# Kernel optimization log

Measured on AMD Instinct MI355X. Metric: run time of the kernel, lower is better.

Reference implementation:

```python
import jax, jax.numpy as jnp
import numpy as np

# Profile-HMM forward-backward in log space.
# inputs : (M, B, L, S) soft/one-hot observation features
# log_A  : (M, Q, Q) row-stochastic log transition matrix
# log_pi : (M, Q)    log initial distribution
# log_B  : (M, Q, S) log emission matrix

M, B, L, Q, S = 1, 64, 2048, 256, 26
EPS = 1e-16


def setup_inputs() -> dict:
    key = jax.random.key(0)
    k1, k2, k3, k4 = jax.random.split(key, 4)
    inputs = jax.random.uniform(k1, (M, B, L, S), dtype=jnp.float32)
    log_A = jax.nn.log_softmax(jax.random.normal(k2, (M, Q, Q), dtype=jnp.float32), axis=-1)
    log_pi = jax.nn.log_softmax(jax.random.normal(k3, (M, Q), dtype=jnp.float32), axis=-1)
    log_B = jax.nn.log_softmax(jax.random.normal(k4, (M, Q, S), dtype=jnp.float32), axis=-1)
    return {"inputs": inputs, "log_A": log_A, "log_pi": log_pi, "log_B": log_B}


def _forward_backward(inputs, log_A, log_pi, log_B):
    # emission probs per state: e[m,b,l,q] = sum_s inputs[m,b,l,s] * B[m,q,s]
    emit = jnp.einsum('mbls,mqs->mblq', inputs, jnp.exp(log_B))
    log_e = jnp.log(emit + EPS)
    log_e_t = jnp.moveaxis(log_e, 2, 0)  # (L, M, B, Q) time-major

    # forward recursion: alpha_t[i] = logsumexp_j(alpha_{t-1}[j] + A[j,i]) + e_t[i]
    alpha0 = log_pi[:, None, :] + log_e_t[0]  # (M, B, Q)

    def fstep(alpha, le):
        new = jax.nn.logsumexp(alpha[..., :, None] + log_A[:, None], axis=-2) + le
        return new, new

    _, alphas = jax.lax.scan(fstep, alpha0, log_e_t[1:])
    alphas = jnp.concatenate([alpha0[None], alphas], axis=0)  # (L, M, B, Q)

    # backward recursion: beta_t[i] = logsumexp_j(A[i,j] + e_{t+1}[j] + beta_{t+1}[j])
    beta_last = jnp.zeros_like(alpha0)

    def bstep(beta, le):
        new = jax.nn.logsumexp(log_A[:, None] + (le + beta)[:, :, None, :], axis=-1)
        return new, new

    _, betas = jax.lax.scan(bstep, beta_last, log_e_t[1:], reverse=True)
    betas = jnp.concatenate([betas, beta_last[None]], axis=0)  # (L, M, B, Q)

    loglik = jax.nn.logsumexp(alphas[-1], axis=-1)  # (M, B)
    post = alphas + betas - loglik[None, :, :, None]  # state posterior log probs
    return jnp.moveaxis(post, 0, 2), loglik  # (M, B, L, Q), (M, B)


def reference(inputs, log_A, log_pi, log_B):
    post, loglik = _forward_backward(inputs, log_A, log_pi, log_B)
    return post, loglik
```

## Files before the change

### kernel.cpp

```cpp
#include <hip/hip_runtime.h>

namespace {

constexpr int B = 64;
constexpr int L = 2048;
constexpr int Q = 256;
constexpr int S = 26;
constexpr float EPS = 1e-16f;
constexpr size_t POST = (size_t)B * L * Q;

typedef _Float16 h2 __attribute__((ext_vector_type(2)));

union U16 {
  uint4 u;
  h2 h[4];
};

struct Smem {
  alignas(16) _Float16 vb[2][Q];
  alignas(16) float rowbuf[2][32];
  float sh[2];
  alignas(16) float afin[Q];
};

__device__ __forceinline__ float wave_max64(float x) {
#pragma unroll
  for (int off = 32; off > 0; off >>= 1) x = fmaxf(x, __shfl_xor(x, off, 64));
  return x;
}
__device__ __forceinline__ float wave_sum64(float x) {
#pragma unroll
  for (int off = 32; off > 0; off >>= 1) x += __shfl_xor(x, off, 64);
  return x;
}

__device__ __forceinline__ float emit_row(const float* __restrict__ rb,
                                          const float* __restrict__ eB) {
  const float4* r4 = (const float4*)rb;
  float4 c0 = r4[0], c1 = r4[1], c2 = r4[2], c3 = r4[3], c4 = r4[4], c5 = r4[5];
  float2 c6 = ((const float2*)rb)[12];
  float a0 = EPS, a1 = 0.f, a2 = 0.f, a3 = 0.f;
  a0 = fmaf(c0.x, eB[0], a0);  a1 = fmaf(c0.y, eB[1], a1);
  a2 = fmaf(c0.z, eB[2], a2);  a3 = fmaf(c0.w, eB[3], a3);
  a0 = fmaf(c1.x, eB[4], a0);  a1 = fmaf(c1.y, eB[5], a1);
  a2 = fmaf(c1.z, eB[6], a2);  a3 = fmaf(c1.w, eB[7], a3);
  a0 = fmaf(c2.x, eB[8], a0);  a1 = fmaf(c2.y, eB[9], a1);
  a2 = fmaf(c2.z, eB[10], a2); a3 = fmaf(c2.w, eB[11], a3);
  a0 = fmaf(c3.x, eB[12], a0); a1 = fmaf(c3.y, eB[13], a1);
  a2 = fmaf(c3.z, eB[14], a2); a3 = fmaf(c3.w, eB[15], a3);
  a0 = fmaf(c4.x, eB[16], a0); a1 = fmaf(c4.y, eB[17], a1);
  a2 = fmaf(c4.z, eB[18], a2); a3 = fmaf(c4.w, eB[19], a3);
  a0 = fmaf(c5.x, eB[20], a0); a1 = fmaf(c5.y, eB[21], a1);
  a2 = fmaf(c5.z, eB[22], a2); a3 = fmaf(c5.w, eB[23], a3);
  a0 = fmaf(c6.x, eB[24], a0); a1 = fmaf(c6.y, eB[25], a1);
  return (a0 + a1) + (a2 + a3);
}

__device__ __forceinline__ float matvec_f16(const h2* __restrict__ Af,
                                            const _Float16* __restrict__ vrow) {
  const uint4* v4 = (const uint4*)vrow;
  float acc[8] = {0.f, 0.f, 0.f, 0.f, 0.f, 0.f, 0.f, 0.f};
#pragma unroll
  for (int c = 0; c < 16; ++c) {
    U16 u;
    u.u = v4[c];
#pragma unroll
    for (int k = 0; k < 4; ++k) {
      const int j = 4 * c + k;
      acc[j & 7] = __builtin_amdgcn_fdot2(u.h[k], Af[j], acc[j & 7], false);
    }
  }
  float s = ((acc[0] + acc[1]) + (acc[2] + acc[3])) +
            ((acc[4] + acc[5]) + (acc[6] + acc[7]));
  return s + __shfl_xor(s, 32, 64);
}

__device__ __forceinline__ void fwd_impl(int b, const float* __restrict__ inputs,
                                         const float* __restrict__ log_A,
                                         const float* __restrict__ log_pi,
                                         const float* __restrict__ log_B,
                                         float* __restrict__ out, Smem& sm) {
  const int tid = threadIdx.x, w = tid >> 6, lane = tid & 63;
  const int l31 = lane & 31;
  const bool lo = lane < 32;
  const int r = w * 32 + l31;
  const int jbase = lo ? 0 : 128;
  const bool stg = (w == 0) && (lane < 13);

  h2 Af[64];
#pragma unroll
  for (int k = 0; k < 64; ++k) {
    float x0 = __expf(log_A[(size_t)(jbase + 2 * k) * Q + r]);
    float x1 = __expf(log_A[(size_t)(jbase + 2 * k + 1) * Q + r]);
    Af[k] = h2{(_Float16)x0, (_Float16)x1};
  }
  float eB[S];
#pragma unroll
  for (int s = 0; s < S; ++s) eB[s] = __expf(log_B[r * S + s]);

  const float2* __restrict__ inp2 = (const float2*)(inputs + (size_t)b * L * S);
  float* __restrict__ post_b = out + (size_t)b * L * Q;

  if (stg) {
    float2 g0 = inp2[lane];
    float2 g1 = inp2[13 + lane];
    ((float2*)sm.rowbuf[1])[lane] = g0;
    ((float2*)sm.rowbuf[0])[lane] = g1;
  }
  __syncthreads();
  float emit0 = emit_row(sm.rowbuf[1], eB);
  float alpha_cur = __logf(emit0) + log_pi[r];
  if (tid == 0) sm.sh[0] = alpha_cur;
  __syncthreads();
  float rd_prev = sm.sh[0];
  if (lo) sm.vb[0][r] = (_Float16)__expf(alpha_cur - rd_prev);
  float alpha_prev = alpha_cur;
  __syncthreads();

  int p = 0;
  for (int t = 1; t < L; ++t) {
    const float rd = sm.sh[p];
    float2 g;
    const int tt = (t + 1 < L) ? t + 1 : L - 1;
    if (stg) g = inp2[(size_t)tt * 13 + lane];
    if (lo) post_b[(size_t)(t - 1) * Q + r] = alpha_prev;
    const float emit = emit_row(sm.rowbuf[p], eB);
    const float X = matvec_f16(Af, sm.vb[p] + jbase);
    const float z = X * emit;
    const float gam = __expf(rd_prev - rd);
    if (lo) sm.vb[p ^ 1][r] = (_Float16)(z * gam);
    alpha_cur = __logf(z) + rd_prev;
    if (tid == 0) sm.sh[p ^ 1] = alpha_cur;
    if (stg) ((float2*)sm.rowbuf[p ^ 1])[lane] = g;
    alpha_prev = alpha_cur;
    rd_prev = rd;
    __syncthreads();
    p ^= 1;
  }

  if (lo) post_b[(size_t)(L - 1) * Q + r] = alpha_prev;
  if (lo) sm.afin[r] = alpha_prev;
  __syncthreads();
  if (w == 0) {
    float4 fa = ((const float4*)sm.afin)[lane];
    float m = fmaxf(fmaxf(fa.x, fa.y), fmaxf(fa.z, fa.w));
    m = wave_max64(m);
    float ss = __expf(fa.x - m) + __expf(fa.y - m) + __expf(fa.z - m) + __expf(fa.w - m);
    ss = wave_sum64(ss);
    if (lane == 0) out[POST + b] = __logf(ss) + m;
  }
}

template <int MODE>
__device__ __forceinline__ void bwd_impl(int b, const float* __restrict__ inputs,
                                         const float* __restrict__ log_A,
                                         const float* __restrict__ log_B,
                                         float* __restrict__ out,
                                         float* __restrict__ ws, Smem& sm) {
  const int tid = threadIdx.x, w = tid >> 6, lane = tid & 63;
  const int l31 = lane & 31;
  const bool lo = lane < 32;
  const int r = w * 32 + l31;
  const int jbase = lo ? 0 : 128;
  const bool stg = (w == 0) && (lane < 13);

  h2 Af[64];
  {
    const float* row = log_A + (size_t)r * Q + jbase;
#pragma unroll
    for (int k = 0; k < 64; ++k) {
      float x0 = __expf(row[2 * k]);
      float x1 = __expf(row[2 * k + 1]);
      Af[k] = h2{(_Float16)x0, (_Float16)x1};
    }
  }
  float eB[S];
#pragma unroll
  for (int s = 0; s < S; ++s) eB[s] = __expf(log_B[r * S + s]);

  const float2* __restrict__ inp2 = (const float2*)(inputs + (size_t)b * L * S);
  float* __restrict__ post_b = out + (size_t)b * L * Q;
  float* __restrict__ ws_b = ws + (size_t)b * L * Q;

  float ll = 0.f, aprev_hold = 0.f;
  if (MODE == 1) {
    ll = out[POST + b];
    aprev_hold = post_b[(size_t)(L - 1) * Q + r];
  }

  if (stg) {
    float2 g0 = inp2[(size_t)(L - 1) * 13 + lane];
    float2 g1 = inp2[(size_t)(L - 2) * 13 + lane];
    ((float2*)sm.rowbuf[1])[lane] = g0;
    ((float2*)sm.rowbuf[0])[lane] = g1;
  }
  __syncthreads();
  float emitL = emit_row(sm.rowbuf[1], eB);
  if (tid == 0) sm.sh[0] = __logf(emitL);
  __syncthreads();
  float rd_prev = sm.sh[0];
  if (lo) sm.vb[0][r] = (_Float16)(emitL * __expf(-rd_prev));
  float beta_prev = 0.f;
  __syncthreads();

  int p = 0;
  for (int t = L - 2; t >= 0; --t) {
    const float rd = sm.sh[p];
    float2 g;
    const int tt = (t > 0) ? t - 1 : 0;
    if (stg) g = inp2[(size_t)tt * 13 + lane];
    float anext = 0.f;
    if (MODE == 0) {
      if (lo) ws_b[(size_t)(t + 1) * Q + r] = beta_prev;
    } else {
      if (lo) post_b[(size_t)(t + 1) * Q + r] = aprev_hold + beta_prev - ll;
      anext = post_b[(size_t)t * Q + r];
    }
    const float emit = emit_row(sm.rowbuf[p], eB);
    const float raw = matvec_f16(Af, sm.vb[p] + jbase);
    const float beta = __logf(raw) + rd_prev;
    const float z = raw * emit;
    const float gam = __expf(rd_prev - rd);
    if (lo) sm.vb[p ^ 1][r] = (_Float16)(z * gam);
    if (tid == 0) sm.sh[p ^ 1] = beta + __logf(emit);
    if (stg) ((float2*)sm.rowbuf[p ^ 1])[lane] = g;
    beta_prev = beta;
    rd_prev = rd;
    if (MODE == 1) aprev_hold = anext;
    __syncthreads();
    p ^= 1;
  }

  if (MODE == 0) {
    if (lo) ws_b[r] = beta_prev;
  } else {
    if (lo) post_b[r] = aprev_hold + beta_prev - ll;
  }
}

__global__ __launch_bounds__(512, 1)
void hmm_fwdbwd(const float* __restrict__ inputs, const float* __restrict__ log_A,
                const float* __restrict__ log_pi, const float* __restrict__ log_B,
                float* __restrict__ out, float* __restrict__ ws) {
  __shared__ Smem sm;
  if (blockIdx.x < B) fwd_impl(blockIdx.x, inputs, log_A, log_pi, log_B, out, sm);
  else                bwd_impl<0>(blockIdx.x - B, inputs, log_A, log_B, out, ws, sm);
}

__global__ __launch_bounds__(256)
void hmm_combine(const float* __restrict__ ws, float* __restrict__ out) {
  const size_t idx = (size_t)blockIdx.x * 256 + threadIdx.x;
  const int b = (int)(idx >> 17);
  const float ll = out[POST + b];
  float4 a = ((const float4*)out)[idx];
  const float4 be = ((const float4*)ws)[idx];
  a.x += be.x - ll;
  a.y += be.y - ll;
  a.z += be.z - ll;
  a.w += be.w - ll;
  ((float4*)out)[idx] = a;
}

__global__ __launch_bounds__(512, 1)
void hmm_fwd_only(const float* __restrict__ inputs, const float* __restrict__ log_A,
                  const float* __restrict__ log_pi, const float* __restrict__ log_B,
                  float* __restrict__ out) {
  __shared__ Smem sm;
  fwd_impl(blockIdx.x, inputs, log_A, log_pi, log_B, out, sm);
}

__global__ __launch_bounds__(512, 1)
void hmm_bwd_fused(const float* __restrict__ inputs, const float* __restrict__ log_A,
                   const float* __restrict__ log_B, float* __restrict__ out) {
  __shared__ Smem sm;
  bwd_impl<1>(blockIdx.x, inputs, log_A, log_B, out, nullptr, sm);
}

}

extern "C" void kernel_launch(void* const* d_in, const int* in_sizes, int n_in,
                              void* d_out, int out_size, void* d_ws, size_t ws_size,
                              hipStream_t stream) {
  const float* inputs = (const float*)d_in[0];
  const float* log_A  = (const float*)d_in[1];
  const float* log_pi = (const float*)d_in[2];
  const float* log_B  = (const float*)d_in[3];
  float* out = (float*)d_out;
  float* ws  = (float*)d_ws;

  if (ws_size >= POST * sizeof(float)) {
    hipLaunchKernelGGL(hmm_fwdbwd, dim3(2 * B), dim3(512), 0, stream,
                       inputs, log_A, log_pi, log_B, out, ws);
    hipLaunchKernelGGL(hmm_combine, dim3((unsigned)(POST / 4 / 256)), dim3(256), 0, stream,
                       ws, out);
  } else {
    hipLaunchKernelGGL(hmm_fwd_only, dim3(B), dim3(512), 0, stream,
                       inputs, log_A, log_pi, log_B, out);
    hipLaunchKernelGGL(hmm_bwd_fused, dim3(B), dim3(512), 0, stream,
                       inputs, log_A, log_B, out);
  }
}
```

Baseline: 1.758 ms.

## Move per-step matvec and emission dot products onto MFMA matrix cores

Replaces the per-lane fdot2 transition matvec and the scalar emission dot product with 16x16x32 f16 MFMA instructions. Each wave now handles 32 states as two 16-column tiles, with only one row of the A operand populated. The emission product uses a hi/lo f16 split to keep near-fp32 accuracy. Launch bounds are raised to two blocks per CU. This trades a wasteful MFMA (only one of 16 rows useful) and extra fragment reads from LDS for shorter per-step latency on the serial recurrence. f16 rounding of the observation inputs also adds some accuracy risk.

```diff
diff --git a/kernel.cpp b/kernel.cpp
--- a/kernel.cpp
+++ b/kernel.cpp
@@ -10,15 +10,15 @@
 constexpr size_t POST = (size_t)B * L * Q;
 
 typedef _Float16 h2 __attribute__((ext_vector_type(2)));
-
-union U16 {
-  uint4 u;
-  h2 h[4];
-};
+typedef _Float16 f16x8 __attribute__((ext_vector_type(8)));
+typedef float f32x4 __attribute__((ext_vector_type(4)));
+
+#define MFMA16(a, b, c) __builtin_amdgcn_mfma_f32_16x16x32_f16((a), (b), (c), 0, 0, 0)
 
 struct Smem {
   alignas(16) _Float16 vb[2][Q];
-  alignas(16) float rowbuf[2][32];
+  alignas(16) _Float16 rowh[2][32];
+  alignas(16) _Float16 rowl[2][32];
   float sh[2];
   alignas(16) float afin[Q];
 };
@@ -34,45 +34,71 @@
   return x;
 }
 
-__device__ __forceinline__ float emit_row(const float* __restrict__ rb,
-                                          const float* __restrict__ eB) {
-  const float4* r4 = (const float4*)rb;
-  float4 c0 = r4[0], c1 = r4[1], c2 = r4[2], c3 = r4[3], c4 = r4[4], c5 = r4[5];
-  float2 c6 = ((const float2*)rb)[12];
-  float a0 = EPS, a1 = 0.f, a2 = 0.f, a3 = 0.f;
-  a0 = fmaf(c0.x, eB[0], a0);  a1 = fmaf(c0.y, eB[1], a1);
-  a2 = fmaf(c0.z, eB[2], a2);  a3 = fmaf(c0.w, eB[3], a3);
-  a0 = fmaf(c1.x, eB[4], a0);  a1 = fmaf(c1.y, eB[5], a1);
-  a2 = fmaf(c1.z, eB[6], a2);  a3 = fmaf(c1.w, eB[7], a3);
-  a0 = fmaf(c2.x, eB[8], a0);  a1 = fmaf(c2.y, eB[9], a1);
-  a2 = fmaf(c2.z, eB[10], a2); a3 = fmaf(c2.w, eB[11], a3);
-  a0 = fmaf(c3.x, eB[12], a0); a1 = fmaf(c3.y, eB[13], a1);
-  a2 = fmaf(c3.z, eB[14], a2); a3 = fmaf(c3.w, eB[15], a3);
-  a0 = fmaf(c4.x, eB[16], a0); a1 = fmaf(c4.y, eB[17], a1);
-  a2 = fmaf(c4.z, eB[18], a2); a3 = fmaf(c4.w, eB[19], a3);
-  a0 = fmaf(c5.x, eB[20], a0); a1 = fmaf(c5.y, eB[21], a1);
-  a2 = fmaf(c5.z, eB[22], a2); a3 = fmaf(c5.w, eB[23], a3);
-  a0 = fmaf(c6.x, eB[24], a0); a1 = fmaf(c6.y, eB[25], a1);
-  return (a0 + a1) + (a2 + a3);
-}
-
-__device__ __forceinline__ float matvec_f16(const h2* __restrict__ Af,
-                                            const _Float16* __restrict__ vrow) {
-  const uint4* v4 = (const uint4*)vrow;
-  float acc[8] = {0.f, 0.f, 0.f, 0.f, 0.f, 0.f, 0.f, 0.f};
-#pragma unroll
-  for (int c = 0; c < 16; ++c) {
-    U16 u;
-    u.u = v4[c];
-#pragma unroll
-    for (int k = 0; k < 4; ++k) {
-      const int j = 4 * c + k;
-      acc[j & 7] = __builtin_amdgcn_fdot2(u.h[k], Af[j], acc[j & 7], false);
-    }
-  }
-  float s = ((acc[0] + acc[1]) + (acc[2] + acc[3])) +
-            ((acc[4] + acc[5]) + (acc[6] + acc[7]));
-  return s + __shfl_xor(s, 32, 64);
+__device__ __forceinline__ void load_emit_frags(const float* __restrict__ log_B,
+                                                int c0, int c1, int g, int q,
+                                                f16x8& Bh0, f16x8& Bl0,
+                                                f16x8& Bh1, f16x8& Bl1) {
+#pragma unroll
+  for (int j = 0; j < 8; ++j) {
+    const int s = g * 8 + j;
+    const float v0 = (s < S) ? __expf(log_B[(size_t)(c0 + q) * S + s]) : 0.f;
+    const float v1 = (s < S) ? __expf(log_B[(size_t)(c1 + q) * S + s]) : 0.f;
+    const _Float16 h0 = (_Float16)v0, h1 = (_Float16)v1;
+    Bh0[j] = h0; Bl0[j] = (_Float16)(v0 - (float)h0);
+    Bh1[j] = h1; Bl1[j] = (_Float16)(v1 - (float)h1);
+  }
+}
+
+__device__ __forceinline__ void stage_row(Smem& sm, int buf, int lane, float2 gg) {
+  _Float16 ah = (_Float16)0.f, bh = (_Float16)0.f;
+  _Float16 al = (_Float16)0.f, bl = (_Float16)0.f;
+  if (lane < 13) {
+    ah = (_Float16)gg.x; bh = (_Float16)gg.y;
+    al = (_Float16)(gg.x - (float)ah);
+    bl = (_Float16)(gg.y - (float)bh);
+  }
+  ((h2*)sm.rowh[buf])[lane] = h2{ah, bh};
+  ((h2*)sm.rowl[buf])[lane] = h2{al, bl};
+}
+
+__device__ __forceinline__ void emit_mfma(const f16x8& xh, const f16x8& xl,
+                                          const f16x8& Bh0, const f16x8& Bl0,
+                                          const f16x8& Bh1, const f16x8& Bl1,
+                                          f32x4& E0, f32x4& E1) {
+  const f32x4 Z = {0.f, 0.f, 0.f, 0.f};
+  E0 = MFMA16(xh, Bl0, Z);
+  E0 = MFMA16(xl, Bh0, E0);
+  E0 = MFMA16(xh, Bh0, E0);
+  E1 = MFMA16(xh, Bl1, Z);
+  E1 = MFMA16(xl, Bh1, E1);
+  E1 = MFMA16(xh, Bh1, E1);
+}
+
+__device__ __forceinline__ void matvec_mfma(const f16x8* va, const f16x8* T0,
+                                            const f16x8* T1, float& x0, float& x1) {
+  const f32x4 Z = {0.f, 0.f, 0.f, 0.f};
+  f32x4 X0a = MFMA16(va[0], T0[0], Z);
+  f32x4 X1a = MFMA16(va[0], T1[0], Z);
+  f32x4 X0b = MFMA16(va[4], T0[4], Z);
+  f32x4 X1b = MFMA16(va[4], T1[4], Z);
+#pragma unroll
+  for (int f = 1; f < 4; ++f) {
+    X0a = MFMA16(va[f], T0[f], X0a);
+    X1a = MFMA16(va[f], T1[f], X1a);
+    X0b = MFMA16(va[f + 4], T0[f + 4], X0b);
+    X1b = MFMA16(va[f + 4], T1[f + 4], X1b);
+  }
+  x0 = X0a[0] + X0b[0];
+  x1 = X1a[0] + X1b[0];
+}
+
+__device__ __forceinline__ void read_frags(Smem& sm, int p, int g,
+                                           f16x8& xh, f16x8& xl, f16x8* va) {
+  xh = *(const f16x8*)(sm.rowh[p] + g * 8);
+  xl = *(const f16x8*)(sm.rowl[p] + g * 8);
+  const _Float16* vbp = sm.vb[p];
+#pragma unroll
+  for (int f = 0; f < 8; ++f) va[f] = *(const f16x8*)(vbp + f * 32 + g * 8);
 }
 
 __device__ __forceinline__ void fwd_impl(int b, const float* __restrict__ inputs,
@@ -81,65 +107,103 @@
                                          const float* __restrict__ log_B,
                                          float* __restrict__ out, Smem& sm) {
   const int tid = threadIdx.x, w = tid >> 6, lane = tid & 63;
-  const int l31 = lane & 31;
-  const bool lo = lane < 32;
-  const int r = w * 32 + l31;
-  const int jbase = lo ? 0 : 128;
-  const bool stg = (w == 0) && (lane < 13);
-
-  h2 Af[64];
-#pragma unroll
-  for (int k = 0; k < 64; ++k) {
-    float x0 = __expf(log_A[(size_t)(jbase + 2 * k) * Q + r]);
-    float x1 = __expf(log_A[(size_t)(jbase + 2 * k + 1) * Q + r]);
-    Af[k] = h2{(_Float16)x0, (_Float16)x1};
-  }
-  float eB[S];
-#pragma unroll
-  for (int s = 0; s < S; ++s) eB[s] = __expf(log_B[r * S + s]);
+  const int g = lane >> 4, q = lane & 15;
+  const int c0 = w * 32, c1 = c0 + 16;
+  const bool rdl = (q == 0);
+  const bool epi = (lane < 16);
+  const bool stg = (w == 0) && (lane < 16);
+
+  f16x8 T0[8], T1[8];
+#pragma unroll
+  for (int f = 0; f < 8; ++f) {
+#pragma unroll
+    for (int j = 0; j < 8; ++j) {
+      const int k = f * 32 + g * 8 + j;
+      T0[f][j] = (_Float16)__expf(log_A[(size_t)k * Q + c0 + q]);
+      T1[f][j] = (_Float16)__expf(log_A[(size_t)k * Q + c1 + q]);
+    }
+  }
+  f16x8 Bh0, Bl0, Bh1, Bl1;
+  load_emit_frags(log_B, c0, c1, g, q, Bh0, Bl0, Bh1, Bl1);
 
   const float2* __restrict__ inp2 = (const float2*)(inputs + (size_t)b * L * S);
   float* __restrict__ post_b = out + (size_t)b * L * Q;
 
   if (stg) {
-    float2 g0 = inp2[lane];
-    float2 g1 = inp2[13 + lane];
-    ((float2*)sm.rowbuf[1])[lane] = g0;
-    ((float2*)sm.rowbuf[0])[lane] = g1;
-  }
-  __syncthreads();
-  float emit0 = emit_row(sm.rowbuf[1], eB);
-  float alpha_cur = __logf(emit0) + log_pi[r];
-  if (tid == 0) sm.sh[0] = alpha_cur;
+    float2 g0, g1;
+    if (lane < 13) { g0 = inp2[lane]; g1 = inp2[13 + lane]; }
+    stage_row(sm, 1, lane, g0);
+    stage_row(sm, 0, lane, g1);
+  }
+  __syncthreads();
+
+  f16x8 xh = {}, xl = {};
+  f16x8 va[8];
+#pragma unroll
+  for (int f = 0; f < 8; ++f) va[f] = f16x8{};
+
+  if (rdl) {
+    xh = *(const f16x8*)(sm.rowh[1] + g * 8);
+    xl = *(const f16x8*)(sm.rowl[1] + g * 8);
+  }
+  f32x4 E0, E1;
+  emit_mfma(xh, xl, Bh0, Bl0, Bh1, Bl1, E0, E1);
+  float zh0 = 1.f, zh1 = 1.f, rdp_h = 0.f;
+  if (epi) {
+    zh0 = (E0[0] + EPS) * __expf(log_pi[c0 + lane]);
+    zh1 = (E1[0] + EPS) * __expf(log_pi[c1 + lane]);
+  }
+  if (tid == 0) sm.sh[0] = __logf(zh0);
   __syncthreads();
   float rd_prev = sm.sh[0];
-  if (lo) sm.vb[0][r] = (_Float16)__expf(alpha_cur - rd_prev);
-  float alpha_prev = alpha_cur;
+  if (epi) {
+    const float sc = __expf(-rd_prev);
+    sm.vb[0][c0 + lane] = (_Float16)(zh0 * sc);
+    sm.vb[0][c1 + lane] = (_Float16)(zh1 * sc);
+  }
   __syncthreads();
 
   int p = 0;
   for (int t = 1; t < L; ++t) {
     const float rd = sm.sh[p];
-    float2 g;
+    float2 gg;
     const int tt = (t + 1 < L) ? t + 1 : L - 1;
-    if (stg) g = inp2[(size_t)tt * 13 + lane];
-    if (lo) post_b[(size_t)(t - 1) * Q + r] = alpha_prev;
-    const float emit = emit_row(sm.rowbuf[p], eB);
-    const float X = matvec_f16(Af, sm.vb[p] + jbase);
-    const float z = X * emit;
+    if (w == 0 && lane < 13) gg = inp2[(size_t)tt * 13 + lane];
+    if (epi) {
+      const float a0 = __logf(zh0) + rdp_h;
+      const float a1 = __logf(zh1) + rdp_h;
+      post_b[(size_t)(t - 1) * Q + c0 + lane] = a0;
+      post_b[(size_t)(t - 1) * Q + c1 + lane] = a1;
+    }
+    if (rdl) read_frags(sm, p, g, xh, xl, va);
+    f32x4 E0_, E1_;
+    emit_mfma(xh, xl, Bh0, Bl0, Bh1, Bl1, E0_, E1_);
+    float x0, x1;
+    matvec_mfma(va, T0, T1, x0, x1);
     const float gam = __expf(rd_prev - rd);
-    if (lo) sm.vb[p ^ 1][r] = (_Float16)(z * gam);
-    alpha_cur = __logf(z) + rd_prev;
-    if (tid == 0) sm.sh[p ^ 1] = alpha_cur;
-    if (stg) ((float2*)sm.rowbuf[p ^ 1])[lane] = g;
-    alpha_prev = alpha_cur;
+    if (epi) {
+      const float e0 = E0_[0] + EPS, e1 = E1_[0] + EPS;
+      const float z0 = x0 * e0, z1 = x1 * e1;
+      sm.vb[p ^ 1][c0 + lane] = (_Float16)(z0 * gam);
+      sm.vb[p ^ 1][c1 + lane] = (_Float16)(z1 * gam);
+      if (tid == 0) sm.sh[p ^ 1] = __logf(z0) + rd_prev;
+      zh0 = z0; zh1 = z1;
+    }
+    rdp_h = rd_prev;
     rd_prev = rd;
+    if (stg) stage_row(sm, p ^ 1, lane, gg);
     __syncthreads();
     p ^= 1;
   }
 
-  if (lo) post_b[(size_t)(L - 1) * Q + r] = alpha_prev;
-  if (lo) sm.afin[r] = alpha_prev;
+  if (epi) {
+    const float a0 = __logf(zh0) + rdp_h;
+    const float a1 = __logf(zh1) + rdp_h;
+    post_b[(size_t)(L - 1) * Q + c0 + lane] = a0;
+    post_b[(size_t)(L - 1) * Q + c1 + lane] = a1;
+    sm.afin[c0 + lane] = a0;
+    sm.afin[c1 + lane] = a1;
+  }
   __syncthreads();
   if (w == 0) {
     float4 fa = ((const float4*)sm.afin)[lane];
@@ -158,87 +222,127 @@
                                          float* __restrict__ out,
                                          float* __restrict__ ws, Smem& sm) {
   const int tid = threadIdx.x, w = tid >> 6, lane = tid & 63;
-  const int l31 = lane & 31;
-  const bool lo = lane < 32;
-  const int r = w * 32 + l31;
-  const int jbase = lo ? 0 : 128;
-  const bool stg = (w == 0) && (lane < 13);
-
-  h2 Af[64];
-  {
-    const float* row = log_A + (size_t)r * Q + jbase;
-#pragma unroll
-    for (int k = 0; k < 64; ++k) {
-      float x0 = __expf(row[2 * k]);
-      float x1 = __expf(row[2 * k + 1]);
-      Af[k] = h2{(_Float16)x0, (_Float16)x1};
-    }
-  }
-  float eB[S];
-#pragma unroll
-  for (int s = 0; s < S; ++s) eB[s] = __expf(log_B[r * S + s]);
+  const int g = lane >> 4, q = lane & 15;
+  const int c0 = w * 32, c1 = c0 + 16;
+  const bool rdl = (q == 0);
+  const bool epi = (lane < 16);
+  const bool stg = (w == 0) && (lane < 16);
+
+  f16x8 T0[8], T1[8];
+#pragma unroll
+  for (int f = 0; f < 8; ++f) {
+#pragma unroll
+    for (int j = 0; j < 8; ++j) {
+      const int k = f * 32 + g * 8 + j;
+      T0[f][j] = (_Float16)__expf(log_A[(size_t)(c0 + q) * Q + k]);
+      T1[f][j] = (_Float16)__expf(log_A[(size_t)(c1 + q) * Q + k]);
+    }
+  }
+  f16x8 Bh0, Bl0, Bh1, Bl1;
+  load_emit_frags(log_B, c0, c1, g, q, Bh0, Bl0, Bh1, Bl1);
 
   const float2* __restrict__ inp2 = (const float2*)(inputs + (size_t)b * L * S);
   float* __restrict__ post_b = out + (size_t)b * L * Q;
   float* __restrict__ ws_b = ws + (size_t)b * L * Q;
 
-  float ll = 0.f, aprev_hold = 0.f;
+  float ll = 0.f, a_h0 = 0.f, a_h1 = 0.f;
   if (MODE == 1) {
     ll = out[POST + b];
-    aprev_hold = post_b[(size_t)(L - 1) * Q + r];
+    if (epi) {
+      a_h0 = post_b[(size_t)(L - 1) * Q + c0 + lane];
+      a_h1 = post_b[(size_t)(L - 1) * Q + c1 + lane];
+    }
   }
 
   if (stg) {
-    float2 g0 = inp2[(size_t)(L - 1) * 13 + lane];
-    float2 g1 = inp2[(size_t)(L - 2) * 13 + lane];
-    ((float2*)sm.rowbuf[1])[lane] = g0;
-    ((float2*)sm.rowbuf[0])[lane] = g1;
-  }
-  __syncthreads();
-  float emitL = emit_row(sm.rowbuf[1], eB);
-  if (tid == 0) sm.sh[0] = __logf(emitL);
+    float2 g0, g1;
+    if (lane < 13) {
+      g0 = inp2[(size_t)(L - 1) * 13 + lane];
+      g1 = inp2[(size_t)(L - 2) * 13 + lane];
+    }
+    stage_row(sm, 1, lane, g0);
+    stage_row(sm, 0, lane, g1);
+  }
+  __syncthreads();
+
+  f16x8 xh = {}, xl = {};
+  f16x8 va[8];
+#pragma unroll
+  for (int f = 0; f < 8; ++f) va[f] = f16x8{};
+
+  if (rdl) {
+    xh = *(const f16x8*)(sm.rowh[1] + g * 8);
+    xl = *(const f16x8*)(sm.rowl[1] + g * 8);
+  }
+  f32x4 E0, E1;
+  emit_mfma(xh, xl, Bh0, Bl0, Bh1, Bl1, E0, E1);
+  float e0i = 1.f, e1i = 1.f;
+  if (epi) { e0i = E0[0] + EPS; e1i = E1[0] + EPS; }
+  if (tid == 0) sm.sh[0] = __logf(e0i);
   __syncthreads();
   float rd_prev = sm.sh[0];
-  if (lo) sm.vb[0][r] = (_Float16)(emitL * __expf(-rd_prev));
-  float beta_prev = 0.f;
+  if (epi) {
+    const float sc = __expf(-rd_prev);
+    sm.vb[0][c0 + lane] = (_Float16)(e0i * sc);
+    sm.vb[0][c1 + lane] = (_Float16)(e1i * sc);
+  }
+  float rh0 = 1.f, rh1 = 1.f, rdp_h = 0.f;
   __syncthreads();
 
   int p = 0;
   for (int t = L - 2; t >= 0; --t) {
     const float rd = sm.sh[p];
-    float2 g;
+    float2 gg;
     const int tt = (t > 0) ? t - 1 : 0;
-    if (stg) g = inp2[(size_t)tt * 13 + lane];
-    float anext = 0.f;
-    if (MODE == 0) {
-      if (lo) ws_b[(size_t)(t + 1) * Q + r] = beta_prev;
-    } else {
-      if (lo) post_b[(size_t)(t + 1) * Q + r] = aprev_hold + beta_prev - ll;
-      anext = post_b[(size_t)t * Q + r];
-    }
-    const float emit = emit_row(sm.rowbuf[p], eB);
-    const float raw = matvec_f16(Af, sm.vb[p] + jbase);
-    const float beta = __logf(raw) + rd_prev;
-    const float z = raw * emit;
+    if (w == 0 && lane < 13) gg = inp2[(size_t)tt * 13 + lane];
+    if (epi) {
+      const float b0 = __logf(rh0) + rdp_h;
+      const float b1 = __logf(rh1) + rdp_h;
+      if (MODE == 0) {
+        ws_b[(size_t)(t + 1) * Q + c0 + lane] = b0;
+        ws_b[(size_t)(t + 1) * Q + c1 + lane] = b1;
+      } else {
+        post_b[(size_t)(t + 1) * Q + c0 + lane] = a_h0 + b0 - ll;
+        post_b[(size_t)(t + 1) * Q + c1 + lane] = a_h1 + b1 - ll;
+        a_h0 = post_b[(size_t)t * Q + c0 + lane];
+        a_h1 = post_b[(size_t)t * Q + c1 + lane];
+      }
+    }
+    if (rdl) read_frags(sm, p, g, xh, xl, va);
+    f32x4 E0_, E1_;
+    emit_mfma(xh, xl, Bh0, Bl0, Bh1, Bl1, E0_, E1_);
+    float r0, r1;
+    matvec_mfma(va, T0, T1, r0, r1);
     const float gam = __expf(rd_prev - rd);
-    if (lo) sm.vb[p ^ 1][r] = (_Float16)(z * gam);
-    if (tid == 0) sm.sh[p ^ 1] = beta + __logf(emit);
-    if (stg) ((float2*)sm.rowbuf[p ^ 1])[lane] = g;
-    beta_prev = beta;
+    if (epi) {
+      const float e0 = E0_[0] + EPS, e1 = E1_[0] + EPS;
+      const float z0 = r0 * e0, z1 = r1 * e1;
+      sm.vb[p ^ 1][c0 + lane] = (_Float16)(z0 * gam);
+      sm.vb[p ^ 1][c1 + lane] = (_Float16)(z1 * gam);
+      if (tid == 0) sm.sh[p ^ 1] = __logf(z0) + rd_prev;
+      rh0 = r0; rh1 = r1;
+    }
+    rdp_h = rd_prev;
     rd_prev = rd;
-    if (MODE == 1) aprev_hold = anext;
+    if (stg) stage_row(sm, p ^ 1, lane, gg);
     __syncthreads();
     p ^= 1;
   }
 
-  if (MODE == 0) {
-    if (lo) ws_b[r] = beta_prev;
-  } else {
-    if (lo) post_b[r] = aprev_hold + beta_prev - ll;
-  }
-}
-
-__global__ __launch_bounds__(512, 1)
+  if (epi) {
+    const float b0 = __logf(rh0) + rdp_h;
+    const float b1 = __logf(rh1) + rdp_h;
+    if (MODE == 0) {
+      ws_b[c0 + lane] = b0;
+      ws_b[c1 + lane] = b1;
+    } else {
+      post_b[c0 + lane] = a_h0 + b0 - ll;
+      post_b[c1 + lane] = a_h1 + b1 - ll;
+    }
+  }
+}
+
+__global__ __launch_bounds__(512, 2)
 void hmm_fwdbwd(const float* __restrict__ inputs, const float* __restrict__ log_A,
                 const float* __restrict__ log_pi, const float* __restrict__ log_B,
                 float* __restrict__ out, float* __restrict__ ws) {
@@ -261,7 +365,7 @@
   ((float4*)out)[idx] = a;
 }
 
-__global__ __launch_bounds__(512, 1)
+__global__ __launch_bounds__(512, 2)
 void hmm_fwd_only(const float* __restrict__ inputs, const float* __restrict__ log_A,
                   const float* __restrict__ log_pi, const float* __restrict__ log_B,
                   float* __restrict__ out) {
@@ -269,7 +373,7 @@
   fwd_impl(blockIdx.x, inputs, log_A, log_pi, log_B, out, sm);
 }
 
-__global__ __launch_bounds__(512, 1)
+__global__ __launch_bounds__(512, 2)
 void hmm_bwd_fused(const float* __restrict__ inputs, const float* __restrict__ log_A,
                    const float* __restrict__ log_B, float* __restrict__ out) {
   __shared__ Smem sm;
```

Measured after the change: 1.630 ms. 1.08x faster.
